# Performance work log

Hardware: AMD Instinct MI355X
Metric: run time of the kernel (lower is better)

Reference implementation:

```python
import jax, jax.numpy as jnp
import numpy as np

AGENT_TYPE_VEHICLE = 1
AGENT_TYPE_PEDESTRIAN = 2
N_VEHICLE_INTENTIONS = 6
N_PEDESTRIAN_INTENTIONS = 2
INTENTION_LOGIT_DIM = 6


def setup_inputs() -> dict:
    key = jax.random.key(0)
    ks = jax.random.split(key, 10)
    B, N, D = 32, 2048, 512
    H = D // 2
    s_in = 1.0 / np.sqrt(D)
    s_h = 1.0 / np.sqrt(H)
    return {
        "repr3": jax.random.normal(ks[0], (B, N, D), dtype=jnp.float32),
        "agent_type_ids": jax.random.randint(ks[1], (B, N), 0, 4, dtype=jnp.int64),
        # vehicle head: Linear(D, D//2) -> GELU -> Linear(D//2, 6)
        "vW1": jax.random.normal(ks[2], (H, D), dtype=jnp.float32) * s_in,
        "vb1": jax.random.normal(ks[3], (H,), dtype=jnp.float32) * s_in,
        "vW2": jax.random.normal(ks[4], (N_VEHICLE_INTENTIONS, H), dtype=jnp.float32) * s_h,
        "vb2": jax.random.normal(ks[5], (N_VEHICLE_INTENTIONS,), dtype=jnp.float32) * s_h,
        # pedestrian head: Linear(D, D//2) -> GELU -> Linear(D//2, 2)
        "pW1": jax.random.normal(ks[6], (H, D), dtype=jnp.float32) * s_in,
        "pb1": jax.random.normal(ks[7], (H,), dtype=jnp.float32) * s_in,
        "pW2": jax.random.normal(ks[8], (N_PEDESTRIAN_INTENTIONS, H), dtype=jnp.float32) * s_h,
        "pb2": jax.random.normal(ks[9], (N_PEDESTRIAN_INTENTIONS,), dtype=jnp.float32) * s_h,
    }


def _mlp(x, W1, b1, W2, b2):
    # x: [B,N,D] -> [B,N,out]; exact (erf) GELU matches torch nn.GELU()
    h = jax.nn.gelu(jnp.einsum("bnd,hd->bnh", x, W1) + b1, approximate=False)
    return jnp.einsum("bnh,oh->bno", h, W2) + b2


def reference(repr3, agent_type_ids, vW1, vb1, vW2, vb2, pW1, pb1, pW2, pb2):
    v_mask = agent_type_ids == AGENT_TYPE_VEHICLE  # [B,N]
    p_mask = agent_type_ids == AGENT_TYPE_PEDESTRIAN
    v_logits = _mlp(repr3, vW1, vb1, vW2, vb2)  # [B,N,6]
    p_logits = _mlp(repr3, pW1, pb1, pW2, pb2)  # [B,N,2]
    pad = INTENTION_LOGIT_DIM - N_PEDESTRIAN_INTENTIONS
    p_padded = jnp.pad(p_logits, ((0, 0), (0, 0), (0, pad)))  # [B,N,6]
    zero = jnp.zeros((), dtype=repr3.dtype)
    intention_logits = (
        jnp.where(v_mask[..., None], v_logits, zero)
        + jnp.where(p_mask[..., None], p_padded, zero)
    )
    return intention_logits, v_mask, p_mask
```

## Files before the change

### kernel.cpp

```cpp
#include <hip/hip_runtime.h>
#include <hip/hip_bf16.h>
#include <math.h>


#define TOKENS 65536
#define DIM    512
#define HID    256
#define ASTR   40
#define ABUFB  5120
#define HSTR   264

using short8 = __attribute__((ext_vector_type(8))) short;
using f32x4  = __attribute__((ext_vector_type(4))) float;

#define BAR()                                                      \
    do {                                                           \
        __builtin_amdgcn_sched_barrier(0);                         \
        asm volatile("s_waitcnt lgkmcnt(0)" ::: "memory");         \
        __builtin_amdgcn_s_barrier();                              \
        __builtin_amdgcn_sched_barrier(0);                         \
    } while (0)

__device__ __forceinline__ unsigned int pkrne(float a, float b) {
    unsigned int ua = __float_as_uint(a);
    unsigned int ub = __float_as_uint(b);
    ua += 0x7FFFu + ((ua >> 16) & 1u);
    ub += 0x7FFFu + ((ub >> 16) & 1u);
    return __builtin_amdgcn_perm(ub, ua, 0x07060302u);
}

__device__ __forceinline__ uint2 cvt4(f32x4 v) {
    return make_uint2(pkrne(v[0], v[1]), pkrne(v[2], v[3]));
}

__device__ __forceinline__ __hip_bfloat16 bf16rne(float x) {
    unsigned int u = __float_as_uint(x);
    u += 0x7FFFu + ((u >> 16) & 1u);
    unsigned short hs = (unsigned short)(u >> 16);
    return *(__hip_bfloat16*)&hs;
}

__device__ __forceinline__ float gelu_exact(float x) {
    const float z  = fabsf(x) * 0.7071067811865475f;
    const float t  = __builtin_amdgcn_rcpf(fmaf(0.3275911f, z, 1.0f));
    float p = fmaf(1.061405429f, t, -1.453152027f);
    p = fmaf(p, t, 1.421413741f);
    p = fmaf(p, t, -0.284496736f);
    p = fmaf(p, t, 0.254829592f);
    p = p * t;
    const float e  = __expf(-z * z);
    const float er = fmaf(-p, e, 1.0f);
    return 0.5f * x * (1.0f + copysignf(er, x));
}

__global__ __launch_bounds__(256)
void prep_kernel(const float* __restrict__ vW1, const float* __restrict__ pW1,
                 const float* __restrict__ vW2, const float* __restrict__ pW2,
                 __hip_bfloat16* __restrict__ Wc, __hip_bfloat16* __restrict__ W2c)
{
    const int i = blockIdx.x * 256 + threadIdx.x;
    if (i < 65536) {
        const int flat = i * 4;
        f32x4 v = (flat < 131072) ? *(const f32x4*)(vW1 + flat)
                                  : *(const f32x4*)(pW1 + flat - 131072);
        *(uint2*)(Wc + flat) = cvt4(v);
    } else if (i < 65536 + 2048) {
        const int flat = (i - 65536) * 4;
        const int row = flat >> 8, col = flat & 255;
        f32x4 v = (f32x4){0.f, 0.f, 0.f, 0.f};
        if (row < 6)                      v = *(const f32x4*)(vW2 + row * HID + col);
        else if (row >= 16 && row < 18)   v = *(const f32x4*)(pW2 + (row - 16) * HID + col);
        *(uint2*)(W2c + flat) = cvt4(v);
    }
}

__global__ __launch_bounds__(256, 3)
void intention_heads_kernel(const float* __restrict__ X,
                            const int* __restrict__ ids,
                            const __hip_bfloat16* __restrict__ Wc,
                            const __hip_bfloat16* __restrict__ W2c,
                            const float* __restrict__ vb1,
                            const float* __restrict__ pb1,
                            const float* __restrict__ vb2,
                            const float* __restrict__ pb2,
                            float* __restrict__ out)
{
    __shared__ __align__(16) unsigned char smem[64 * HSTR * 2];
    __hip_bfloat16* H = (__hip_bfloat16*)smem;

    const int cpx = gridDim.x >> 3;
    const int bid = (blockIdx.x & 7) * cpx + (blockIdx.x >> 3);

    const int head = bid & 1;
    const int row0 = (bid >> 1) * 64;

    const int tid  = threadIdx.x;
    const int wave = tid >> 6;
    const int lane = tid & 63;
    const int quad = lane >> 4;
    const int l16  = lane & 15;
    const int wcol = wave * 64;

    const int q  = tid & 7;
    const int r2 = tid >> 3;
    const float* Xs = X + (long)(row0 + r2) * DIM + q * 4;

    const __hip_bfloat16* Wrow[4];
    #pragma unroll
    for (int j = 0; j < 4; ++j)
        Wrow[j] = Wc + (long)(head * 256 + wcol + j * 16 + l16) * DIM + quad * 8;

    f32x4 acc[4][4];
    #pragma unroll
    for (int i = 0; i < 4; ++i)
        #pragma unroll
        for (int j = 0; j < 4; ++j)
            acc[i][j] = (f32x4){0.f, 0.f, 0.f, 0.f};

    f32x4 ga0 = *(const f32x4*)(Xs);
    f32x4 ga1 = *(const f32x4*)(Xs + 32 * DIM);
    f32x4 gb0 = *(const f32x4*)(Xs + 32);
    f32x4 gb1 = *(const f32x4*)(Xs + 32 * DIM + 32);
    {
        __hip_bfloat16* A = (__hip_bfloat16*)smem;
        *(uint2*)&A[r2 * ASTR + q * 4]        = cvt4(ga0);
        *(uint2*)&A[(r2 + 32) * ASTR + q * 4] = cvt4(ga1);
    }
    BAR();
    ga0 = gb0; ga1 = gb1;

    #pragma unroll
    for (int it = 0; it < DIM / 32; ++it) {
        __hip_bfloat16* cur = (__hip_bfloat16*)(smem + (it % 3) * ABUFB);
        __hip_bfloat16* nxt = (__hip_bfloat16*)(smem + ((it + 1) % 3) * ABUFB);

        if (it < 14) {
            gb0 = *(const f32x4*)(Xs + (it + 2) * 32);
            gb1 = *(const f32x4*)(Xs + 32 * DIM + (it + 2) * 32);
        }

        short8 bc[4];
        #pragma unroll
        for (int j = 0; j < 4; ++j)
            bc[j] = *(const short8*)(Wrow[j] + it * 32);

        short8 af[4];
        #pragma unroll
        for (int i = 0; i < 4; ++i)
            af[i] = *(const short8*)&cur[(i * 16 + l16) * ASTR + quad * 8];

        #pragma unroll
        for (int i = 0; i < 4; ++i)
            #pragma unroll
            for (int j = 0; j < 4; ++j)
                acc[i][j] = __builtin_amdgcn_mfma_f32_16x16x32_bf16(af[i], bc[j], acc[i][j], 0, 0, 0);

        if (it < 15) {
            *(uint2*)&nxt[r2 * ASTR + q * 4]        = cvt4(ga0);
            *(uint2*)&nxt[(r2 + 32) * ASTR + q * 4] = cvt4(ga1);
        }
        BAR();
        ga0 = gb0; ga1 = gb1;
    }

    const float* b1 = head ? pb1 : vb1;
    float b1v[4];
    #pragma unroll
    for (int j = 0; j < 4; ++j)
        b1v[j] = b1[wcol + j * 16 + l16];

    #pragma unroll
    for (int i = 0; i < 4; ++i) {
        #pragma unroll
        for (int j = 0; j < 4; ++j) {
            const int col = wcol + j * 16 + l16;
            #pragma unroll
            for (int rr = 0; rr < 4; ++rr) {
                const int row = i * 16 + quad * 4 + rr;
                H[row * HSTR + col] = bf16rne(gelu_exact(acc[i][j][rr] + b1v[j]));
            }
        }
    }
    BAR();

    const float* b2 = head ? pb2 : vb2;
    const int nOut = head ? 2 : 6;

    f32x4 acc2 = (f32x4){0.f, 0.f, 0.f, 0.f};
    const int tokb = wave * 16;
    const short* hbase  = (const short*)&H[(tokb + l16) * HSTR + quad * 8];
    const __hip_bfloat16* w2base = W2c + (head * 16 + l16) * HID + quad * 8;
    #pragma unroll
    for (int k0 = 0; k0 < HID; k0 += 32) {
        short8 af    = *(const short8*)(hbase + k0);
        short8 bfrag = *(const short8*)(w2base + k0);
        acc2 = __builtin_amdgcn_mfma_f32_16x16x32_bf16(af, bfrag, acc2, 0, 0, 0);
    }

    const float b2v = (l16 < nOut) ? b2[l16] : 0.0f;

    #pragma unroll
    for (int rr = 0; rr < 4; ++rr) {
        const int t = row0 + tokb + quad * 4 + rr;
        const int type = ids[t];
        if (head == 0) {
            if (l16 == 0) {
                out[TOKENS * 6 + t] = (type == 1) ? 1.0f : 0.0f;
                out[TOKENS * 7 + t] = (type == 2) ? 1.0f : 0.0f;
            }
            if (l16 < 6) {
                if (type == 1)
                    out[t * 6 + l16] = acc2[rr] + b2v;
                else if (type != 2)
                    out[t * 6 + l16] = 0.0f;
            }
        } else {
            if (l16 < 6 && type == 2)
                out[t * 6 + l16] = (l16 < 2) ? (acc2[rr] + b2v) : 0.0f;
        }
    }
}

extern "C" void kernel_launch(void* const* d_in, const int* in_sizes, int n_in,
                              void* d_out, int out_size, void* d_ws, size_t ws_size,
                              hipStream_t stream) {
    (void)n_in; (void)out_size; (void)ws_size;
    const float* X   = (const float*)d_in[0];
    const int*   ids = (const int*)d_in[1];
    const float* vW1 = (const float*)d_in[2];
    const float* vb1 = (const float*)d_in[3];
    const float* vW2 = (const float*)d_in[4];
    const float* vb2 = (const float*)d_in[5];
    const float* pW1 = (const float*)d_in[6];
    const float* pb1 = (const float*)d_in[7];
    const float* pW2 = (const float*)d_in[8];
    const float* pb2 = (const float*)d_in[9];
    float* out = (float*)d_out;

    __hip_bfloat16* Wc  = (__hip_bfloat16*)d_ws;
    __hip_bfloat16* W2c = Wc + 512 * DIM;

    hipLaunchKernelGGL(prep_kernel, dim3(264), dim3(256), 0, stream,
                       vW1, pW1, vW2, pW2, Wc, W2c);

    const int tokens = in_sizes[1];
    const int grid   = (tokens / 64) * 2;

    hipLaunchKernelGGL(intention_heads_kernel, dim3(grid), dim3(256), 0, stream,
                       X, ids, Wc, W2c, vb1, pb1, vb2, pb2, out);
}
```

Before: 275.7 us.

## Load X directly from global into MFMA fragments, dropping LDS staging

```diff
diff --git a/kernel.cpp b/kernel.cpp
--- a/kernel.cpp
+++ b/kernel.cpp
@@ -6,20 +6,10 @@
 #define TOKENS 65536
 #define DIM    512
 #define HID    256
-#define ASTR   40
-#define ABUFB  5120
 #define HSTR   264
 
 using short8 = __attribute__((ext_vector_type(8))) short;
 using f32x4  = __attribute__((ext_vector_type(4))) float;
-
-#define BAR()                                                      \
-    do {                                                           \
-        __builtin_amdgcn_sched_barrier(0);                         \
-        asm volatile("s_waitcnt lgkmcnt(0)" ::: "memory");         \
-        __builtin_amdgcn_s_barrier();                              \
-        __builtin_amdgcn_sched_barrier(0);                         \
-    } while (0)
 
 __device__ __forceinline__ unsigned int pkrne(float a, float b) {
     unsigned int ua = __float_as_uint(a);
@@ -74,7 +64,7 @@
     }
 }
 
-__global__ __launch_bounds__(256, 3)
+__global__ __launch_bounds__(256, 4)
 void intention_heads_kernel(const float* __restrict__ X,
                             const int* __restrict__ ids,
                             const __hip_bfloat16* __restrict__ Wc,
@@ -85,8 +75,7 @@
                             const float* __restrict__ pb2,
                             float* __restrict__ out)
 {
-    __shared__ __align__(16) unsigned char smem[64 * HSTR * 2];
-    __hip_bfloat16* H = (__hip_bfloat16*)smem;
+    __shared__ __align__(16) __hip_bfloat16 H[64 * HSTR];
 
     const int cpx = gridDim.x >> 3;
     const int bid = (blockIdx.x & 7) * cpx + (blockIdx.x >> 3);
@@ -101,9 +90,10 @@
     const int l16  = lane & 15;
     const int wcol = wave * 64;
 
-    const int q  = tid & 7;
-    const int r2 = tid >> 3;
-    const float* Xs = X + (long)(row0 + r2) * DIM + q * 4;
+    const float* Xr[4];
+    #pragma unroll
+    for (int i = 0; i < 4; ++i)
+        Xr[i] = X + (long)(row0 + i * 16 + l16) * DIM + quad * 8;
 
     const __hip_bfloat16* Wrow[4];
     #pragma unroll
@@ -117,28 +107,7 @@
         for (int j = 0; j < 4; ++j)
             acc[i][j] = (f32x4){0.f, 0.f, 0.f, 0.f};
 
-    f32x4 ga0 = *(const f32x4*)(Xs);
-    f32x4 ga1 = *(const f32x4*)(Xs + 32 * DIM);
-    f32x4 gb0 = *(const f32x4*)(Xs + 32);
-    f32x4 gb1 = *(const f32x4*)(Xs + 32 * DIM + 32);
-    {
-        __hip_bfloat16* A = (__hip_bfloat16*)smem;
-        *(uint2*)&A[r2 * ASTR + q * 4]        = cvt4(ga0);
-        *(uint2*)&A[(r2 + 32) * ASTR + q * 4] = cvt4(ga1);
-    }
-    BAR();
-    ga0 = gb0; ga1 = gb1;
-
-    #pragma unroll
     for (int it = 0; it < DIM / 32; ++it) {
-        __hip_bfloat16* cur = (__hip_bfloat16*)(smem + (it % 3) * ABUFB);
-        __hip_bfloat16* nxt = (__hip_bfloat16*)(smem + ((it + 1) % 3) * ABUFB);
-
-        if (it < 14) {
-            gb0 = *(const f32x4*)(Xs + (it + 2) * 32);
-            gb1 = *(const f32x4*)(Xs + 32 * DIM + (it + 2) * 32);
-        }
-
         short8 bc[4];
         #pragma unroll
         for (int j = 0; j < 4; ++j)
@@ -146,21 +115,20 @@
 
         short8 af[4];
         #pragma unroll
-        for (int i = 0; i < 4; ++i)
-            af[i] = *(const short8*)&cur[(i * 16 + l16) * ASTR + quad * 8];
+        for (int i = 0; i < 4; ++i) {
+            f32x4 xa = *(const f32x4*)(Xr[i] + it * 32);
+            f32x4 xb = *(const f32x4*)(Xr[i] + it * 32 + 4);
+            union { short8 s; uint2 u[2]; } f;
+            f.u[0] = cvt4(xa);
+            f.u[1] = cvt4(xb);
+            af[i] = f.s;
+        }
 
         #pragma unroll
         for (int i = 0; i < 4; ++i)
             #pragma unroll
             for (int j = 0; j < 4; ++j)
                 acc[i][j] = __builtin_amdgcn_mfma_f32_16x16x32_bf16(af[i], bc[j], acc[i][j], 0, 0, 0);
-
-        if (it < 15) {
-            *(uint2*)&nxt[r2 * ASTR + q * 4]        = cvt4(ga0);
-            *(uint2*)&nxt[(r2 + 32) * ASTR + q * 4] = cvt4(ga1);
-        }
-        BAR();
-        ga0 = gb0; ga1 = gb1;
     }
 
     const float* b1 = head ? pb1 : vb1;
@@ -181,7 +149,7 @@
             }
         }
     }
-    BAR();
+    __syncthreads();
 
     const float* b2 = head ? pb2 : vb2;
     const int nOut = head ? 2 : 6;
```

Result: slower. 354.1 us (+28.4%).

## Pre-swizzle weights into MFMA fragment order for coalesced B loads

Applied to the files above, without the earlier changes.

```diff
diff --git a/kernel.cpp b/kernel.cpp
--- a/kernel.cpp
+++ b/kernel.cpp
@@ -59,22 +59,40 @@
                  __hip_bfloat16* __restrict__ Wc, __hip_bfloat16* __restrict__ W2c)
 {
     const int i = blockIdx.x * 256 + threadIdx.x;
-    if (i < 65536) {
-        const int flat = i * 4;
-        f32x4 v = (flat < 131072) ? *(const f32x4*)(vW1 + flat)
-                                  : *(const f32x4*)(pW1 + flat - 131072);
-        *(uint2*)(Wc + flat) = cvt4(v);
-    } else if (i < 65536 + 2048) {
-        const int flat = (i - 65536) * 4;
-        const int row = flat >> 8, col = flat & 255;
-        f32x4 v = (f32x4){0.f, 0.f, 0.f, 0.f};
-        if (row < 6)                      v = *(const f32x4*)(vW2 + row * HID + col);
-        else if (row >= 16 && row < 18)   v = *(const f32x4*)(pW2 + (row - 16) * HID + col);
-        *(uint2*)(W2c + flat) = cvt4(v);
-    }
-}
-
-__global__ __launch_bounds__(256, 3)
+    if (i < 32768) {
+        const int lane = i & 63;
+        const int it   = (i >> 6) & 15;
+        const int nt   = i >> 10;
+        const int head = nt >> 4;
+        const int row  = (nt & 15) * 16 + (lane & 15);
+        const int k    = it * 32 + (lane >> 4) * 8;
+        const float* src = (head ? pW1 : vW1) + row * DIM + k;
+        f32x4 a = *(const f32x4*)(src);
+        f32x4 b = *(const f32x4*)(src + 4);
+        uint2 lo = cvt4(a), hi = cvt4(b);
+        *(uint4*)((char*)Wc + (long)i * 16) = make_uint4(lo.x, lo.y, hi.x, hi.y);
+    } else if (i < 32768 + 1024) {
+        const int c    = i - 32768;
+        const int lane = c & 63;
+        const int rest = c >> 6;
+        const int head = rest & 1;
+        const int ks   = rest >> 1;
+        const int l16  = lane & 15;
+        const int quad = lane >> 4;
+        const int nOut = head ? 2 : 6;
+        uint4 o = make_uint4(0u, 0u, 0u, 0u);
+        if (l16 < nOut) {
+            const float* src = (head ? pW2 : vW2) + l16 * HID + ks * 32 + quad * 8;
+            f32x4 a = *(const f32x4*)(src);
+            f32x4 b = *(const f32x4*)(src + 4);
+            uint2 lo = cvt4(a), hi = cvt4(b);
+            o = make_uint4(lo.x, lo.y, hi.x, hi.y);
+        }
+        *(uint4*)((char*)W2c + (long)c * 16) = o;
+    }
+}
+
+__global__ __launch_bounds__(256, 4)
 void intention_heads_kernel(const float* __restrict__ X,
                             const int* __restrict__ ids,
                             const __hip_bfloat16* __restrict__ Wc,
@@ -105,10 +123,8 @@
     const int r2 = tid >> 3;
     const float* Xs = X + (long)(row0 + r2) * DIM + q * 4;
 
-    const __hip_bfloat16* Wrow[4];
-    #pragma unroll
-    for (int j = 0; j < 4; ++j)
-        Wrow[j] = Wc + (long)(head * 256 + wcol + j * 16 + l16) * DIM + quad * 8;
+    const char* Bq = (const char*)Wc
+                   + (long)(head * 16 + wave * 4) * 16384 + (long)lane * 16;
 
     f32x4 acc[4][4];
     #pragma unroll
@@ -142,7 +158,7 @@
         short8 bc[4];
         #pragma unroll
         for (int j = 0; j < 4; ++j)
-            bc[j] = *(const short8*)(Wrow[j] + it * 32);
+            bc[j] = *(const short8*)(Bq + j * 16384 + it * 1024);
 
         short8 af[4];
         #pragma unroll
@@ -188,12 +204,12 @@
 
     f32x4 acc2 = (f32x4){0.f, 0.f, 0.f, 0.f};
     const int tokb = wave * 16;
-    const short* hbase  = (const short*)&H[(tokb + l16) * HSTR + quad * 8];
-    const __hip_bfloat16* w2base = W2c + (head * 16 + l16) * HID + quad * 8;
-    #pragma unroll
-    for (int k0 = 0; k0 < HID; k0 += 32) {
-        short8 af    = *(const short8*)(hbase + k0);
-        short8 bfrag = *(const short8*)(w2base + k0);
+    const short* hbase = (const short*)&H[(tokb + l16) * HSTR + quad * 8];
+    const char*  w2q   = (const char*)W2c + head * 1024 + (long)lane * 16;
+    #pragma unroll
+    for (int ks = 0; ks < 8; ++ks) {
+        short8 af    = *(const short8*)(hbase + ks * 32);
+        short8 bfrag = *(const short8*)(w2q + ks * 2048);
         acc2 = __builtin_amdgcn_mfma_f32_16x16x32_bf16(af, bfrag, acc2, 0, 0, 0);
     }
 
@@ -240,7 +256,7 @@
     __hip_bfloat16* Wc  = (__hip_bfloat16*)d_ws;
     __hip_bfloat16* W2c = Wc + 512 * DIM;
 
-    hipLaunchKernelGGL(prep_kernel, dim3(264), dim3(256), 0, stream,
+    hipLaunchKernelGGL(prep_kernel, dim3(132), dim3(256), 0, stream,
                        vW1, pW1, vW2, pW2, Wc, W2c);
 
     const int tokens = in_sizes[1];
```

After: 272.5 us. Within noise of the previous version (-1.2%).
